# Performance work log

Hardware: AMD Instinct MI355X
Metric: run time of the kernel (lower is better)

Reference implementation:

```python
import jax, jax.numpy as jnp
import numpy as np

HIDDEN = 1024
HEADS = 16
HEAD_DIM = HIDDEN // HEADS


def setup_inputs() -> dict:
    key = jax.random.key(0)
    ks = jax.random.split(key, 9)
    s = 1.0 / np.sqrt(HIDDEN)
    inp = {
        "x": jax.random.normal(ks[0], (4, 2048, HIDDEN), dtype=jnp.float32),
        "wq": jax.random.uniform(ks[1], (HIDDEN, HIDDEN), jnp.float32, -s, s),
        "bq": jax.random.uniform(ks[2], (HIDDEN,), jnp.float32, -s, s),
        "wk": jax.random.uniform(ks[3], (HIDDEN, HIDDEN), jnp.float32, -s, s),
        "bk": jax.random.uniform(ks[4], (HIDDEN,), jnp.float32, -s, s),
        "wv": jax.random.uniform(ks[5], (HIDDEN, HIDDEN), jnp.float32, -s, s),
        "bv": jax.random.uniform(ks[6], (HIDDEN,), jnp.float32, -s, s),
        "wo": jax.random.uniform(ks[7], (HIDDEN, HIDDEN), jnp.float32, -s, s),
        "bo": jax.random.uniform(ks[8], (HIDDEN,), jnp.float32, -s, s),
    }
    return inp


def reference(x, wq, bq, wk, bk, wv, bv, wo, bo):
    B, S, D = x.shape
    H, Hd = HEADS, HEAD_DIM
    # torch Linear: y = x @ W.T + b
    def split_heads(t):  # [B,S,D] -> [B,H,S,Hd]
        return t.reshape(B, S, H, Hd).transpose(0, 2, 1, 3)
    q = split_heads(x @ wq.T + bq)
    k = split_heads(x @ wk.T + bk)
    v = split_heads(x @ wv.T + bv)
    scores = jnp.einsum('bhqd,bhkd->bhqk', q, k) / jnp.sqrt(jnp.float32(Hd))
    attn = jax.nn.softmax(scores, axis=-1)  # dropout is identity in eval
    ctx = jnp.einsum('bhqk,bhkd->bhqd', attn, v)
    ctx = ctx.transpose(0, 2, 1, 3).reshape(B, S, D)
    pooled = ctx.mean(axis=1)  # [B, D]
    out = pooled @ wo.T + bo
    return out, attn.mean(axis=1)
```

## Files before the change

### kernel.cpp

```cpp
#include <hip/hip_runtime.h>

#define B_ 4
#define S_ 2048
#define D_ 1024
#define H_ 16
#define HD_ 64
#define M_ 8192

typedef __attribute__((ext_vector_type(8))) short          bf16x8;
typedef __attribute__((ext_vector_type(8))) unsigned short u16x8;
typedef __attribute__((ext_vector_type(4))) float          f32x4;

#define MFMA16(a, b, c) __builtin_amdgcn_mfma_f32_16x16x32_bf16((a), (b), (c), 0, 0, 0)

#define SCL 0.18033688011112042f

__device__ __forceinline__ unsigned short f2b(float f) {
    unsigned int u = __float_as_uint(f);
    return (unsigned short)((u + 0x7fffu + ((u >> 16) & 1u)) >> 16);
}

__device__ __forceinline__ unsigned int cvtpk_bf16(float lo, float hi) {
    unsigned int r;
    asm("v_cvt_pk_bf16_f32 %0, %1, %2" : "=v"(r) : "v"(lo), "v"(hi));
    return r;
}

__device__ __forceinline__ unsigned short* swz64(unsigned short* base, int row, int col) {
    unsigned off = ((unsigned)row << 7) + ((unsigned)col << 1);
    off ^= (unsigned)((row & 7) << 4);
    return (unsigned short*)((char*)base + off);
}

__global__ __launch_bounds__(256) void cast_k(const float* __restrict__ src,
                                              unsigned short* __restrict__ dst, int n) {
    int i = (blockIdx.x * 256 + threadIdx.x) * 4;
    if (i >= n) return;
    float4 v = *(const float4*)(src + i);
    ushort4 o;
    o.x = f2b(v.x); o.y = f2b(v.y); o.z = f2b(v.z); o.w = f2b(v.w);
    *(ushort4*)(dst + i) = o;
}

__global__ __launch_bounds__(256) void cast3_k(
    const float* __restrict__ s0, const float* __restrict__ s1, const float* __restrict__ s2,
    unsigned short* __restrict__ d0, unsigned short* __restrict__ d1,
    unsigned short* __restrict__ d2, int n) {
    const float* src = (blockIdx.y == 0) ? s0 : (blockIdx.y == 1) ? s1 : s2;
    unsigned short* dst = (blockIdx.y == 0) ? d0 : (blockIdx.y == 1) ? d1 : d2;
    int i = (blockIdx.x * 256 + threadIdx.x) * 4;
    if (i >= n) return;
    float4 v = *(const float4*)(src + i);
    ushort4 o;
    o.x = f2b(v.x); o.y = f2b(v.y); o.z = f2b(v.z); o.w = f2b(v.w);
    *(ushort4*)(dst + i) = o;
}

__global__ __launch_bounds__(256) void qkv_gemm_k(
    const unsigned short* __restrict__ xb,
    const unsigned short* __restrict__ wb0, const unsigned short* __restrict__ wb1,
    const unsigned short* __restrict__ wb2,
    const float* __restrict__ bq, const float* __restrict__ bk, const float* __restrict__ bv,
    unsigned short* __restrict__ Qo, unsigned short* __restrict__ Ko,
    unsigned short* __restrict__ VT)
{
    __shared__ unsigned short xs[128][72];
    __shared__ unsigned short wsm[128][72];

    const unsigned short* W; const float* bias;
    if (blockIdx.z == 0)      { W = wb0; bias = bq; }
    else if (blockIdx.z == 1) { W = wb1; bias = bk; }
    else                      { W = wb2; bias = bv; }

    const int m0 = blockIdx.x * 128, n0 = blockIdx.y * 128;
    const int tid = threadIdx.x, lane = tid & 63, wid = tid >> 6;
    const int wm = (wid >> 1) * 64, wn = (wid & 1) * 64;
    const int srow = tid >> 3;
    const int skc  = (tid & 7) * 8;

    f32x4 acc[4][4] = {};

    for (int k0 = 0; k0 < D_; k0 += 64) {
        u16x8 xa[4], wa[4];
        #pragma unroll
        for (int r = 0; r < 4; ++r) {
            int row = srow + 32 * r;
            xa[r] = *(const u16x8*)&xb[(size_t)(m0 + row) * D_ + k0 + skc];
            wa[r] = *(const u16x8*)&W [(size_t)(n0 + row) * D_ + k0 + skc];
        }
        __syncthreads();
        #pragma unroll
        for (int r = 0; r < 4; ++r) {
            int row = srow + 32 * r;
            *(u16x8*)&xs[row][skc]  = xa[r];
            *(u16x8*)&wsm[row][skc] = wa[r];
        }
        __syncthreads();
        #pragma unroll
        for (int kd = 0; kd < 2; ++kd) {
            const int kc = 32 * kd + 8 * (lane >> 4);
            bf16x8 af[4], bfr[4];
            #pragma unroll
            for (int mf = 0; mf < 4; ++mf)
                af[mf] = *(const bf16x8*)&xs[wm + 16 * mf + (lane & 15)][kc];
            #pragma unroll
            for (int nf = 0; nf < 4; ++nf)
                bfr[nf] = *(const bf16x8*)&wsm[wn + 16 * nf + (lane & 15)][kc];
            #pragma unroll
            for (int mf = 0; mf < 4; ++mf)
                #pragma unroll
                for (int nf = 0; nf < 4; ++nf)
                    acc[mf][nf] = MFMA16(af[mf], bfr[nf], acc[mf][nf]);
        }
    }

    const int col_l = lane & 15, rgrp = lane >> 4;
    if (blockIdx.z != 2) {
        unsigned short* out = (blockIdx.z == 0) ? Qo : Ko;
        const float oscale = (blockIdx.z == 0) ? SCL : 1.0f;
        #pragma unroll
        for (int nf = 0; nf < 4; ++nf) {
            const int n = n0 + wn + 16 * nf + col_l;
            const float bval = bias[n];
            const int h = n >> 6, d = n & 63;
            #pragma unroll
            for (int mf = 0; mf < 4; ++mf)
                #pragma unroll
                for (int r = 0; r < 4; ++r) {
                    int m = m0 + wm + 16 * mf + 4 * rgrp + r;
                    int bI = m >> 11, s = m & 2047;
                    out[(((size_t)bI * H_ + h) * S_ + s) * HD_ + d]
                        = f2b((acc[mf][nf][r] + bval) * oscale);
                }
        }
    } else {
        #pragma unroll
        for (int nf = 0; nf < 4; ++nf) {
            const int n = n0 + wn + 16 * nf + col_l;
            const float bval = bias[n];
            const int h = n >> 6, d = n & 63;
            #pragma unroll
            for (int mf = 0; mf < 4; ++mf) {
                int m = m0 + wm + 16 * mf + 4 * rgrp;
                int bI = m >> 11, s = m & 2047;
                ushort4 o;
                o.x = f2b(acc[mf][nf][0] + bval);
                o.y = f2b(acc[mf][nf][1] + bval);
                o.z = f2b(acc[mf][nf][2] + bval);
                o.w = f2b(acc[mf][nf][3] + bval);
                *(ushort4*)&VT[(((size_t)bI * H_ + h) * HD_ + d) * S_ + s] = o;
            }
        }
    }
}

__global__ __launch_bounds__(256) void attn_ctx_k(
    const unsigned short* __restrict__ Q, const unsigned short* __restrict__ K,
    const unsigned short* __restrict__ VT,
    float* __restrict__ Linv, float* __restrict__ PPOOL)
{
    __shared__ unsigned short ks0[64 * 64];
    __shared__ unsigned short vt0[64 * 64];
    __shared__ unsigned short ps0[64 * 64];
    __shared__ float pp[4][64];
    __shared__ float lsm[4][32];

    const int lin = blockIdx.x;
    const int g   = (lin & 7) | ((lin >> 7) << 3);
    const int qb  = (lin >> 3) & 15;
    const int b   = g >> 4, h = g & 15;
    const int q0  = qb * 128;

    const size_t hoff = ((size_t)(b * H_ + h)) * S_ * HD_;
    const unsigned short* Qh  = Q  + hoff;
    const unsigned short* Kh  = K  + hoff;
    const unsigned short* VTh = VT + hoff;

    const int tid = threadIdx.x, lane = tid & 63, wid = tid >> 6;
    const int srow = tid >> 3;
    const int skc  = (tid & 7) * 8;
    const int col_l = lane & 15, rgrp = lane >> 4;

    bf16x8 qf[2][2];
    #pragma unroll
    for (int i = 0; i < 2; ++i)
        #pragma unroll
        for (int kd = 0; kd < 2; ++kd)
            qf[i][kd] = *(const bf16x8*)&Qh[(size_t)(q0 + 32 * wid + 16 * i + col_l) * HD_
                                            + 32 * kd + 8 * rgrp];

    f32x4 cacc[2][4] = {};
    float lp[2] = {};

    for (int kb = 0; kb < S_; kb += 64) {
        u16x8 ka[2], va[2];
        #pragma unroll
        for (int r = 0; r < 2; ++r) {
            int row = srow + 32 * r;
            ka[r] = *(const u16x8*)&Kh [(size_t)(kb + row) * HD_ + skc];
            va[r] = *(const u16x8*)&VTh[(size_t)row * S_ + kb + skc];
        }
        __syncthreads();
        #pragma unroll
        for (int r = 0; r < 2; ++r) {
            int row = srow + 32 * r;
            *(u16x8*)swz64(ks0, row, skc) = ka[r];
            *(u16x8*)swz64(vt0, row, skc) = va[r];
        }
        __syncthreads();

        #pragma unroll
        for (int i = 0; i < 2; ++i) {
            unsigned int w[8];
            #pragma unroll
            for (int n = 0; n < 4; ++n) {
                f32x4 s = {};
                #pragma unroll
                for (int kd = 0; kd < 2; ++kd) {
                    bf16x8 kf = *(const bf16x8*)swz64(ks0, 16 * n + col_l, 32 * kd + 8 * rgrp);
                    s = MFMA16(kf, qf[i][kd], s);
                }
                float e0 = exp2f(s[0]), e1 = exp2f(s[1]);
                float e2 = exp2f(s[2]), e3 = exp2f(s[3]);
                lp[i] += (e0 + e1) + (e2 + e3);
                w[2 * n]     = cvtpk_bf16(e0, e1);
                w[2 * n + 1] = cvtpk_bf16(e2, e3);
            }
            #pragma unroll
            for (int n = 0; n < 4; ++n) {
                uint2 wpair = { w[2 * n], w[2 * n + 1] };
                *(uint2*)swz64(ps0, 16 * wid + col_l, 16 * n + 4 * rgrp) = wpair;
            }
            #pragma unroll
            for (int kk = 0; kk < 2; ++kk) {
                bf16x8 pa = *(const bf16x8*)swz64(ps0, 16 * wid + col_l, 32 * kk + 8 * rgrp);
                #pragma unroll
                for (int nd = 0; nd < 4; ++nd) {
                    bf16x8 vf = *(const bf16x8*)swz64(vt0, 16 * nd + col_l, 32 * kk + 8 * rgrp);
                    cacc[i][nd] = MFMA16(pa, vf, cacc[i][nd]);
                }
            }
        }
    }

    #pragma unroll
    for (int i = 0; i < 2; ++i) {
        float v = lp[i];
        v += __shfl_xor(v, 16); v += __shfl_xor(v, 32);
        lp[i] = v;
    }
    if (lane < 16) {
        #pragma unroll
        for (int i = 0; i < 2; ++i) {
            float inv = 1.0f / lp[i];
            Linv[((size_t)(b * H_ + h)) * S_ + q0 + 32 * wid + 16 * i + lane] = inv;
            lsm[wid][16 * i + lane] = inv;
        }
    }

    float pool4[4] = {};
    #pragma unroll
    for (int i = 0; i < 2; ++i)
        #pragma unroll
        for (int r = 0; r < 4; ++r) {
            float inv = lsm[wid][16 * i + 4 * rgrp + r];
            #pragma unroll
            for (int n = 0; n < 4; ++n)
                pool4[n] = fmaf(cacc[i][n][r], inv, pool4[n]);
        }
    #pragma unroll
    for (int n = 0; n < 4; ++n) {
        float v = pool4[n];
        v += __shfl_xor(v, 16); v += __shfl_xor(v, 32);
        pool4[n] = v;
    }
    if (lane < 16) {
        #pragma unroll
        for (int n = 0; n < 4; ++n) pp[wid][16 * n + lane] = pool4[n];
    }
    __syncthreads();
    if (tid < 64) {
        float s = pp[0][tid] + pp[1][tid] + pp[2][tid] + pp[3][tid];
        PPOOL[((size_t)(b * H_ + h) * (S_ / 128) + qb) * 64 + tid] = s;
    }
}

__global__ __launch_bounds__(256) void attn_mean_k(
    const unsigned short* __restrict__ Q, const unsigned short* __restrict__ K,
    const float* __restrict__ Linv, float* __restrict__ attn_out)
{
    __shared__ unsigned short qs[128][72];
    __shared__ unsigned short ksm[64][72];
    __shared__ float lsm[128];

    const int k0 = blockIdx.x * 64, q0 = blockIdx.y * 128, b = blockIdx.z;
    const int tid = threadIdx.x, lane = tid & 63, wid = tid >> 6;
    const int col_l = lane & 15, rgrp = lane >> 4;
    const int qrow = tid >> 1, qcol = (tid & 1) * 32;
    const int krow = tid >> 2, kcol = (tid & 3) * 16;

    f32x4 macc[4][2] = {};

    for (int h = 0; h < H_; ++h) {
        const size_t hoff = ((size_t)(b * H_ + h)) * S_ * HD_;
        const unsigned short* Qh = Q + hoff;
        const unsigned short* Kh = K + hoff;

        u16x8 qa[4], ka[2];
        #pragma unroll
        for (int j = 0; j < 4; ++j)
            qa[j] = *(const u16x8*)&Qh[(size_t)(q0 + qrow) * HD_ + qcol + 8 * j];
        #pragma unroll
        for (int j = 0; j < 2; ++j)
            ka[j] = *(const u16x8*)&Kh[(size_t)(k0 + krow) * HD_ + kcol + 8 * j];
        float lval = 0.f;
        if (tid < 128) lval = Linv[((size_t)(b * H_ + h)) * S_ + q0 + tid];

        __syncthreads();
        #pragma unroll
        for (int j = 0; j < 4; ++j) *(u16x8*)&qs[qrow][qcol + 8 * j] = qa[j];
        #pragma unroll
        for (int j = 0; j < 2; ++j) *(u16x8*)&ksm[krow][kcol + 8 * j] = ka[j];
        if (tid < 128) lsm[tid] = lval;
        __syncthreads();

        bf16x8 qf[2][2];
        #pragma unroll
        for (int i = 0; i < 2; ++i)
            #pragma unroll
            for (int kd = 0; kd < 2; ++kd)
                qf[i][kd] = *(const bf16x8*)&qs[32 * wid + 16 * i + col_l][32 * kd + 8 * rgrp];

        float li0 = lsm[32 * wid + col_l] * 0.0625f;
        float li1 = lsm[32 * wid + 16 + col_l] * 0.0625f;

        #pragma unroll
        for (int n = 0; n < 4; ++n) {
            f32x4 s0 = {}, s1 = {};
            #pragma unroll
            for (int kd = 0; kd < 2; ++kd) {
                bf16x8 kf = *(const bf16x8*)&ksm[16 * n + col_l][32 * kd + 8 * rgrp];
                s0 = MFMA16(kf, qf[0][kd], s0);
                s1 = MFMA16(kf, qf[1][kd], s1);
            }
            #pragma unroll
            for (int r = 0; r < 4; ++r) {
                macc[n][0][r] = fmaf(exp2f(s0[r]), li0, macc[n][0][r]);
                macc[n][1][r] = fmaf(exp2f(s1[r]), li1, macc[n][1][r]);
            }
        }
    }

    #pragma unroll
    for (int n = 0; n < 4; ++n)
        #pragma unroll
        for (int i = 0; i < 2; ++i) {
            int q = q0 + 32 * wid + 16 * i + col_l;
            *(f32x4*)&attn_out[((size_t)b * S_ + q) * S_ + k0 + 16 * n + 4 * rgrp]
                = macc[n][i];
        }
}

__global__ __launch_bounds__(256) void out_k(
    const float* __restrict__ PPOOL, const float* __restrict__ wo,
    const float* __restrict__ bo, float* __restrict__ out)
{
    __shared__ float psm[D_];
    const int b = blockIdx.x >> 2;
    for (int d = threadIdx.x; d < D_; d += 256) {
        const float* pp = PPOOL + ((size_t)(b * H_ + (d >> 6)) * (S_ / 128)) * 64 + (d & 63);
        float s = 0.f;
        #pragma unroll
        for (int qb = 0; qb < S_ / 128; ++qb) s += pp[qb * 64];
        psm[d] = s * (1.0f / S_);
    }
    __syncthreads();
    const int j = (blockIdx.x & 3) * 256 + threadIdx.x;
    float sum = bo[j];
    const float* wr = wo + (size_t)j * D_;
    for (int d = 0; d < D_; d += 4) {
        float4 w4 = *(const float4*)&wr[d];
        sum += psm[d] * w4.x + psm[d+1] * w4.y + psm[d+2] * w4.z + psm[d+3] * w4.w;
    }
    out[b * D_ + j] = sum;
}

extern "C" void kernel_launch(void* const* d_in, const int* in_sizes, int n_in,
                              void* d_out, int out_size, void* d_ws, size_t ws_size,
                              hipStream_t stream)
{
    const float* x  = (const float*)d_in[0];
    const float* wq = (const float*)d_in[1];
    const float* bq = (const float*)d_in[2];
    const float* wk = (const float*)d_in[3];
    const float* bk = (const float*)d_in[4];
    const float* wv = (const float*)d_in[5];
    const float* bv = (const float*)d_in[6];
    const float* wo = (const float*)d_in[7];
    const float* bo = (const float*)d_in[8];
    float* out = (float*)d_out;

    char* ws = (char*)d_ws;
    const size_t XN  = (size_t)M_ * D_;
    const size_t WN  = (size_t)D_ * D_;
    const size_t QN  = (size_t)B_ * H_ * S_ * HD_;

    unsigned short* xb  = (unsigned short*)ws;                 ws += XN * 2;
    unsigned short* wqb = (unsigned short*)ws;                 ws += WN * 2;
    unsigned short* wkb = (unsigned short*)ws;                 ws += WN * 2;
    unsigned short* wvb = (unsigned short*)ws;                 ws += WN * 2;
    unsigned short* Qb  = (unsigned short*)ws;                 ws += QN * 2;
    unsigned short* Kb  = (unsigned short*)ws;                 ws += QN * 2;
    unsigned short* VTb = (unsigned short*)ws;                 ws += QN * 2;
    float* Lb    = (float*)ws;                                 ws += (size_t)B_ * H_ * S_ * 4;
    float* PPOOL = (float*)ws;

    cast_k<<<dim3(XN / 1024), 256, 0, stream>>>(x, xb, (int)XN);
    cast3_k<<<dim3(WN / 1024, 3), 256, 0, stream>>>(wq, wk, wv, wqb, wkb, wvb, (int)WN);

    qkv_gemm_k<<<dim3(M_ / 128, D_ / 128, 3), 256, 0, stream>>>(
        xb, wqb, wkb, wvb, bq, bk, bv, Qb, Kb, VTb);
    attn_ctx_k<<<dim3(1024), 256, 0, stream>>>(Qb, Kb, VTb, Lb, PPOOL);
    attn_mean_k<<<dim3(S_ / 64, S_ / 128, B_), 256, 0, stream>>>(Qb, Kb, Lb, out + B_ * D_);
    out_k<<<16, 256, 0, stream>>>(PPOOL, wo, bo, out);
}
```

Before: 426.7 us.

## Switch attention context kernel to 32x32 MFMA with register-resident P

Rewrites the attention-context inner loop to use 32x32x16 bf16 MFMAs, computing S^T tiles so the exponentiated probabilities stay in registers in the right layout to feed the PV MFMA directly. This drops the shared-memory staging buffer for P and its write/read round trip. It also cuts the number of MFMA issues and K/V fragment loads per tile. V fragments are now assembled from two 4-element LDS reads, and the accumulator layout changes, which raises register pressure and needs a reworked pooling and row-sum reduction.

```diff
diff --git a/kernel.cpp b/kernel.cpp
--- a/kernel.cpp
+++ b/kernel.cpp
@@ -7,11 +7,14 @@
 #define HD_ 64
 #define M_ 8192
 
-typedef __attribute__((ext_vector_type(8))) short          bf16x8;
-typedef __attribute__((ext_vector_type(8))) unsigned short u16x8;
-typedef __attribute__((ext_vector_type(4))) float          f32x4;
+typedef __attribute__((ext_vector_type(8)))  short          bf16x8;
+typedef __attribute__((ext_vector_type(4)))  short          s16x4;
+typedef __attribute__((ext_vector_type(8)))  unsigned short u16x8;
+typedef __attribute__((ext_vector_type(4)))  float          f32x4;
+typedef __attribute__((ext_vector_type(16))) float          f32x16;
 
 #define MFMA16(a, b, c) __builtin_amdgcn_mfma_f32_16x16x32_bf16((a), (b), (c), 0, 0, 0)
+#define MFMA32(a, b, c) __builtin_amdgcn_mfma_f32_32x32x16_bf16((a), (b), (c), 0, 0, 0)
 
 #define SCL 0.18033688011112042f
 
@@ -161,17 +164,16 @@
 {
     __shared__ unsigned short ks0[64 * 64];
     __shared__ unsigned short vt0[64 * 64];
-    __shared__ unsigned short ps0[64 * 64];
     __shared__ float pp[4][64];
     __shared__ float lsm[4][32];
 
     const int lin = blockIdx.x;
     const int g   = (lin & 7) | ((lin >> 7) << 3);
     const int qb  = (lin >> 3) & 15;
-    const int b   = g >> 4, h = g & 15;
+    const int b   = g >> 4, h_ = g & 15;
     const int q0  = qb * 128;
 
-    const size_t hoff = ((size_t)(b * H_ + h)) * S_ * HD_;
+    const size_t hoff = ((size_t)(b * H_ + h_)) * S_ * HD_;
     const unsigned short* Qh  = Q  + hoff;
     const unsigned short* Kh  = K  + hoff;
     const unsigned short* VTh = VT + hoff;
@@ -179,18 +181,15 @@
     const int tid = threadIdx.x, lane = tid & 63, wid = tid >> 6;
     const int srow = tid >> 3;
     const int skc  = (tid & 7) * 8;
-    const int col_l = lane & 15, rgrp = lane >> 4;
-
-    bf16x8 qf[2][2];
+    const int l31 = lane & 31, h = lane >> 5;
+
+    bf16x8 qf[4];
     #pragma unroll
-    for (int i = 0; i < 2; ++i)
-        #pragma unroll
-        for (int kd = 0; kd < 2; ++kd)
-            qf[i][kd] = *(const bf16x8*)&Qh[(size_t)(q0 + 32 * wid + 16 * i + col_l) * HD_
-                                            + 32 * kd + 8 * rgrp];
-
-    f32x4 cacc[2][4] = {};
-    float lp[2] = {};
+    for (int kd = 0; kd < 4; ++kd)
+        qf[kd] = *(const bf16x8*)&Qh[(size_t)(q0 + 32 * wid + l31) * HD_ + 16 * kd + 8 * h];
+
+    f32x16 cacc[2] = {};
+    float lp = 0.f;
 
     for (int kb = 0; kb < S_; kb += 64) {
         u16x8 ka[2], va[2];
@@ -210,78 +209,63 @@
         __syncthreads();
 
         #pragma unroll
-        for (int i = 0; i < 2; ++i) {
-            unsigned int w[8];
-            #pragma unroll
-            for (int n = 0; n < 4; ++n) {
-                f32x4 s = {};
+        for (int kr = 0; kr < 2; ++kr) {
+            f32x16 sacc = {};
+            #pragma unroll
+            for (int kd = 0; kd < 4; ++kd) {
+                bf16x8 kf = *(const bf16x8*)swz64(ks0, 32 * kr + l31, 16 * kd + 8 * h);
+                sacc = MFMA32(kf, qf[kd], sacc);
+            }
+            float e[16];
+            #pragma unroll
+            for (int m = 0; m < 16; ++m) e[m] = exp2f(sacc[m]);
+            #pragma unroll
+            for (int m = 0; m < 16; m += 4)
+                lp += (e[m] + e[m + 1]) + (e[m + 2] + e[m + 3]);
+            unsigned int pk[8];
+            #pragma unroll
+            for (int j = 0; j < 8; ++j) pk[j] = cvtpk_bf16(e[2 * j], e[2 * j + 1]);
+
+            #pragma unroll
+            for (int db = 0; db < 2; ++db) {
+                const int d = 32 * db + l31;
                 #pragma unroll
-                for (int kd = 0; kd < 2; ++kd) {
-                    bf16x8 kf = *(const bf16x8*)swz64(ks0, 16 * n + col_l, 32 * kd + 8 * rgrp);
-                    s = MFMA16(kf, qf[i][kd], s);
-                }
-                float e0 = exp2f(s[0]), e1 = exp2f(s[1]);
-                float e2 = exp2f(s[2]), e3 = exp2f(s[3]);
-                lp[i] += (e0 + e1) + (e2 + e3);
-                w[2 * n]     = cvtpk_bf16(e0, e1);
-                w[2 * n + 1] = cvtpk_bf16(e2, e3);
-            }
-            #pragma unroll
-            for (int n = 0; n < 4; ++n) {
-                uint2 wpair = { w[2 * n], w[2 * n + 1] };
-                *(uint2*)swz64(ps0, 16 * wid + col_l, 16 * n + 4 * rgrp) = wpair;
-            }
-            #pragma unroll
-            for (int kk = 0; kk < 2; ++kk) {
-                bf16x8 pa = *(const bf16x8*)swz64(ps0, 16 * wid + col_l, 32 * kk + 8 * rgrp);
-                #pragma unroll
-                for (int nd = 0; nd < 4; ++nd) {
-                    bf16x8 vf = *(const bf16x8*)swz64(vt0, 16 * nd + col_l, 32 * kk + 8 * rgrp);
-                    cacc[i][nd] = MFMA16(pa, vf, cacc[i][nd]);
+                for (int ks = 0; ks < 2; ++ks) {
+                    s16x4 vlo = *(const s16x4*)swz64(vt0, d, 32 * kr + 16 * ks + 4 * h);
+                    s16x4 vhi = *(const s16x4*)swz64(vt0, d, 32 * kr + 16 * ks + 8 + 4 * h);
+                    bf16x8 vb = __builtin_shufflevector(vlo, vhi, 0, 1, 2, 3, 4, 5, 6, 7);
+                    union { unsigned int u[4]; bf16x8 v; } af;
+                    af.u[0] = pk[4 * ks + 0]; af.u[1] = pk[4 * ks + 1];
+                    af.u[2] = pk[4 * ks + 2]; af.u[3] = pk[4 * ks + 3];
+                    cacc[db] = MFMA32(af.v, vb, cacc[db]);
                 }
             }
         }
     }
 
+    lp += __shfl_xor(lp, 32);
+    if (lane < 32) {
+        float inv = 1.0f / lp;
+        Linv[((size_t)(b * H_ + h_)) * S_ + q0 + 32 * wid + lane] = inv;
+        lsm[wid][lane] = inv;
+    }
+
+    float poold[2] = {};
     #pragma unroll
-    for (int i = 0; i < 2; ++i) {
-        float v = lp[i];
-        v += __shfl_xor(v, 16); v += __shfl_xor(v, 32);
-        lp[i] = v;
-    }
-    if (lane < 16) {
-        #pragma unroll
-        for (int i = 0; i < 2; ++i) {
-            float inv = 1.0f / lp[i];
-            Linv[((size_t)(b * H_ + h)) * S_ + q0 + 32 * wid + 16 * i + lane] = inv;
-            lsm[wid][16 * i + lane] = inv;
-        }
-    }
-
-    float pool4[4] = {};
+    for (int db = 0; db < 2; ++db)
+        #pragma unroll
+        for (int m = 0; m < 16; ++m)
+            poold[db] = fmaf(cacc[db][m], lsm[wid][(m & 3) + 8 * (m >> 2) + 4 * h],
+                             poold[db]);
     #pragma unroll
-    for (int i = 0; i < 2; ++i)
-        #pragma unroll
-        for (int r = 0; r < 4; ++r) {
-            float inv = lsm[wid][16 * i + 4 * rgrp + r];
-            #pragma unroll
-            for (int n = 0; n < 4; ++n)
-                pool4[n] = fmaf(cacc[i][n][r], inv, pool4[n]);
-        }
-    #pragma unroll
-    for (int n = 0; n < 4; ++n) {
-        float v = pool4[n];
-        v += __shfl_xor(v, 16); v += __shfl_xor(v, 32);
-        pool4[n] = v;
-    }
-    if (lane < 16) {
-        #pragma unroll
-        for (int n = 0; n < 4; ++n) pp[wid][16 * n + lane] = pool4[n];
+    for (int db = 0; db < 2; ++db) {
+        poold[db] += __shfl_xor(poold[db], 32);
+        if (lane < 32) pp[wid][32 * db + lane] = poold[db];
     }
     __syncthreads();
     if (tid < 64) {
         float s = pp[0][tid] + pp[1][tid] + pp[2][tid] + pp[3][tid];
-        PPOOL[((size_t)(b * H_ + h) * (S_ / 128) + qb) * 64 + tid] = s;
+        PPOOL[((size_t)(b * H_ + h_) * (S_ / 128) + qb) * 64 + tid] = s;
     }
 }
 
```

New measurement: 417.0 us. -2.3%, faster.
